# Kernel tuning notes

Measured on AMD Instinct MI355X. Metric: run time of the kernel, lower is better.

Reference implementation:

```python
import jax, jax.numpy as jnp
import numpy as np

HEADS = 16
S = 1024      # affine_dim
B, L = 4, 2048


def _conv1x1(x, W, b):
    # Conv1d with kernel_size=1: pointwise channel mixing. x: (B, C, L)
    return jnp.einsum('oc,bcl->bol', W, x) + b[None, :, None]


def setup_inputs() -> dict:
    key = jax.random.key(0)
    ks = jax.random.split(key, 7)
    scale = 1.0 / np.sqrt(S)  # ~ torch Conv1d default init scale
    return {
        'x':  jax.random.normal(ks[0], (B, S, L), dtype=jnp.float32),
        'Wk': jax.random.normal(ks[1], (S, S), dtype=jnp.float32) * scale,
        'bk': jax.random.normal(ks[2], (S,), dtype=jnp.float32) * scale,
        'Wq': jax.random.normal(ks[3], (S, S), dtype=jnp.float32) * scale,
        'bq': jax.random.normal(ks[4], (S,), dtype=jnp.float32) * scale,
        'Wp': jax.random.normal(ks[5], (S, S), dtype=jnp.float32) * scale,
        'bp': jax.random.normal(ks[6], (S,), dtype=jnp.float32) * scale,
    }


def reference(x, Wk, bk, Wq, bq, Wp, bp):
    b, c, l = x.shape
    h = HEADS
    d = c // h
    keys = _conv1x1(x, Wk, bk).reshape(b, h, d, l)
    queries = _conv1x1(x, Wq, bq).reshape(b, h, d, l)
    # scores[b,h,i,j] = sum_d keys[...,d,i] * queries[...,d,j]  (keys^T @ queries)
    # NOTE: original scales by `seqlen ** 1 / 2` == seqlen / 2 (Python precedence),
    # i.e. multiply by 2/L, NOT 1/sqrt(L). Faithfully preserved.
    scores = jnp.einsum('bhdi,bhdj->bhij', keys, queries) * (2.0 / l)
    attn = jax.nn.softmax(scores, axis=-1)
    xh = x.reshape(b, h, d, l)  # raw x used as values
    out = jnp.einsum('bhdi,bhij->bhdj', xh, attn).reshape(b, c, l)
    return _conv1x1(out, Wp, bp)
```

## Files before the change

kernel.cpp:

```cpp
#include <hip/hip_runtime.h>
#include <hip/hip_bf16.h>
#include <cstdint>
#include <cstddef>

#ifndef __has_builtin
#define __has_builtin(x) 0
#endif

#define DEVI __device__ __forceinline__

typedef __attribute__((ext_vector_type(8))) __bf16 bf16x8;
typedef __attribute__((ext_vector_type(4))) float float4v;
typedef __attribute__((ext_vector_type(16))) float float16v;
typedef __attribute__((ext_vector_type(4))) unsigned short ushort4v;
typedef __attribute__((ext_vector_type(4))) unsigned int uint4v;

constexpr int Bd = 4, Sd = 1024, Ld = 2048, Hd = 16, Dd = 64;

DEVI unsigned short f2bf(float x){
  union { float f; unsigned u; } v; v.f = x;
  unsigned r = v.u + 0x7fffu + ((v.u >> 16) & 1u);
  return (unsigned short)(r >> 16);
}

DEVI unsigned pack2(float lo, float hi){
  union { float f; unsigned u; } a, b; a.f = lo; b.f = hi;
  unsigned ra = a.u + 0x8000u;
  unsigned rb = b.u + 0x8000u;
#if __has_builtin(__builtin_amdgcn_perm)
  return __builtin_amdgcn_perm(rb, ra, 0x07060302u);
#else
  return (ra >> 16) | (rb & 0xffff0000u);
#endif
}

DEVI float fast_exp2(float x){
#if __has_builtin(__builtin_amdgcn_exp2f)
  return __builtin_amdgcn_exp2f(x);
#else
  return exp2f(x);
#endif
}

DEVI void plane32_swap(unsigned &a, unsigned &b){
  asm("v_permlane32_swap_b32 %0, %1" : "+v"(a), "+v"(b));
}

DEVI void gload_lds16(const void* g, void* lds){
  __builtin_amdgcn_global_load_lds(
      (const __attribute__((address_space(1))) void*)g,
      (__attribute__((address_space(3))) void*)lds,
      16, 0, 0);
}

DEVI float4v mfma_bf16(bf16x8 a, bf16x8 b, float4v c){
  return __builtin_amdgcn_mfma_f32_16x16x32_bf16(a, b, c, 0, 0, 0);
}

DEVI float16v mfma32_bf16(bf16x8 a, bf16x8 b, float16v c){
  return __builtin_amdgcn_mfma_f32_32x32x16_bf16(a, b, c, 0, 0, 0);
}


__global__ void wcast_kernel(const float* __restrict__ Wk, const float* __restrict__ Wq,
                             const float* __restrict__ Wp,
                             unsigned short* __restrict__ Wkbf, unsigned short* __restrict__ Wqbf,
                             unsigned short* __restrict__ Wpbf, float ck){
  size_t i = ((size_t)blockIdx.x * 256 + threadIdx.x) * 4;
  float4v a = *(const float4v*)(Wk + i);
  float4v b = *(const float4v*)(Wq + i);
  float4v c = *(const float4v*)(Wp + i);
  ushort4v oa = { f2bf(a[0]*ck), f2bf(a[1]*ck), f2bf(a[2]*ck), f2bf(a[3]*ck) };
  ushort4v ob = { f2bf(b[0]), f2bf(b[1]), f2bf(b[2]), f2bf(b[3]) };
  ushort4v oc = { f2bf(c[0]), f2bf(c[1]), f2bf(c[2]), f2bf(c[3]) };
  *(ushort4v*)(Wkbf + i) = oa;
  *(ushort4v*)(Wqbf + i) = ob;
  *(ushort4v*)(Wpbf + i) = oc;
}

__global__ void transpose_cast(const float* __restrict__ x, unsigned short* __restrict__ Xt){
  __shared__ float tile[32][33];
  const int b = blockIdx.z;
  const int l0 = blockIdx.x * 32;
  const int s0 = blockIdx.y * 32;
  const int t = threadIdx.x;
  {
    const int r = t >> 3, c4 = (t & 7) * 4;
    float4v v = *(const float4v*)(x + ((size_t)b*Sd + s0 + r)*Ld + l0 + c4);
    tile[r][c4+0] = v[0]; tile[r][c4+1] = v[1];
    tile[r][c4+2] = v[2]; tile[r][c4+3] = v[3];
  }
  __syncthreads();
  {
    const int l = t >> 3, g4 = (t & 7) * 4;
    ushort4v o = { f2bf(tile[g4+0][l]), f2bf(tile[g4+1][l]),
                   f2bf(tile[g4+2][l]), f2bf(tile[g4+3][l]) };
    *(ushort4v*)(Xt + ((size_t)b*Ld + l0 + l)*Sd + s0 + g4) = o;
  }
}

template<int OUT_MODE>
__global__ __launch_bounds__(256, 2)
void conv_gemm(const unsigned short* __restrict__ A,
               const unsigned short* __restrict__ Bt,
               const float* __restrict__ bias, float bscale,
               unsigned short* __restrict__ outT,
               float* __restrict__ outF)
{
  constexpr int BK = 32;
  constexpr int NKSTEP = Sd / BK;
  __shared__ __attribute__((aligned(16))) unsigned short Abuf[2][128*BK];
  __shared__ __attribute__((aligned(16))) unsigned short Bbuf[2][128*BK];

  const int b  = blockIdx.z;
  const int n0 = blockIdx.x * 128;
  const int m0 = blockIdx.y * 128;
  const int tid = threadIdx.x;
  const int w = tid >> 6, lane = tid & 63, lr = lane & 15, lg = lane >> 4;
  const int wm = (w >> 1) * 64, wn = (w & 1) * 64;

  const unsigned short* Abase = A + (size_t)m0 * Sd;
  const unsigned short* Bbase = Bt + ((size_t)b * Ld + n0) * Sd;

  auto stage = [&](int bf, int kt){
    #pragma unroll
    for (int p = 0; p < 2; ++p){
      int slot = p*256 + tid;
      int row = slot >> 2, c = slot & 3;
      int csrc = c ^ ((row >> 1) & 3);
      gload_lds16(Abase + (size_t)row * Sd + kt*BK + csrc*8,
                  (void*)(&Abuf[bf][(size_t)(p*256 + w*64) * 8]));
    }
    #pragma unroll
    for (int p = 0; p < 2; ++p){
      int slot = p*256 + tid;
      int row = slot >> 2, c = slot & 3;
      int csrc = c ^ ((row >> 1) & 3);
      gload_lds16(Bbase + (size_t)row * Sd + kt*BK + csrc*8,
                  (void*)(&Bbuf[bf][(size_t)(p*256 + w*64) * 8]));
    }
  };

  const int gsw = lg ^ ((lr >> 1) & 3);

  float4v acc[4][4];
  #pragma unroll
  for (int i = 0; i < 4; ++i)
    #pragma unroll
    for (int j = 0; j < 4; ++j)
      acc[i][j] = (float4v){0.f, 0.f, 0.f, 0.f};

  stage(0, 0);
  __syncthreads();
  int cur = 0;
  for (int kt = 0; kt < NKSTEP; ++kt){
    if (kt + 1 < NKSTEP) stage(cur ^ 1, kt + 1);
    bf16x8 af[4], bfv[4];
    #pragma unroll
    for (int i = 0; i < 4; ++i){
      int row = wm + i*16 + lr;
      af[i] = *(const bf16x8*)((const char*)&Abuf[cur][0] + (size_t)row*64 + gsw*16);
    }
    #pragma unroll
    for (int j = 0; j < 4; ++j){
      int row = wn + j*16 + lr;
      bfv[j] = *(const bf16x8*)((const char*)&Bbuf[cur][0] + (size_t)row*64 + gsw*16);
    }
    #pragma unroll
    for (int i = 0; i < 4; ++i)
      #pragma unroll
      for (int j = 0; j < 4; ++j)
        acc[i][j] = mfma_bf16(af[i], bfv[j], acc[i][j]);
    __syncthreads();
    cur ^= 1;
  }

  #pragma unroll
  for (int i = 0; i < 4; ++i){
    const int mb = m0 + wm + i*16 + lg*4;
    float4v bv = *(const float4v*)(bias + mb);
    #pragma unroll
    for (int j = 0; j < 4; ++j){
      const int n = n0 + wn + j*16 + lr;
      float4v v = acc[i][j];
      float o0 = v[0] + bscale*bv[0];
      float o1 = v[1] + bscale*bv[1];
      float o2 = v[2] + bscale*bv[2];
      float o3 = v[3] + bscale*bv[3];
      if (OUT_MODE == 0){
        ushort4v o = { f2bf(o0), f2bf(o1), f2bf(o2), f2bf(o3) };
        *(ushort4v*)(outT + ((size_t)b*Ld + n)*Sd + mb) = o;
      } else {
        outF[((size_t)b*Sd + mb + 0)*Ld + n] = o0;
        outF[((size_t)b*Sd + mb + 1)*Ld + n] = o1;
        outF[((size_t)b*Sd + mb + 2)*Ld + n] = o2;
        outF[((size_t)b*Sd + mb + 3)*Ld + n] = o3;
      }
    }
  }
}

__global__ __launch_bounds__(256, 2)
void conv_gemm_kq(const unsigned short* __restrict__ Ak,
                  const unsigned short* __restrict__ Aq,
                  const unsigned short* __restrict__ Bt,
                  const float* __restrict__ bk, const float* __restrict__ bq,
                  float ck,
                  unsigned short* __restrict__ Kt,
                  unsigned short* __restrict__ Qt)
{
  constexpr int BK = 32;
  constexpr int NKSTEP = Sd / BK;
  __shared__ __attribute__((aligned(16))) unsigned short AbufK[2][128*BK];
  __shared__ __attribute__((aligned(16))) unsigned short AbufQ[2][128*BK];
  __shared__ __attribute__((aligned(16))) unsigned short Bbuf[2][128*BK];

  const int b  = blockIdx.z;
  const int n0 = blockIdx.x * 128;
  const int m0 = blockIdx.y * 128;
  const int tid = threadIdx.x;
  const int w = tid >> 6, lane = tid & 63, lr = lane & 15, lg = lane >> 4;
  const int wm = (w >> 1) * 64, wn = (w & 1) * 64;

  const unsigned short* AKbase = Ak + (size_t)m0 * Sd;
  const unsigned short* AQbase = Aq + (size_t)m0 * Sd;
  const unsigned short* Bbase  = Bt + ((size_t)b * Ld + n0) * Sd;

  auto stage = [&](int bf, int kt){
    #pragma unroll
    for (int p = 0; p < 2; ++p){
      int slot = p*256 + tid;
      int row = slot >> 2, c = slot & 3;
      int csrc = c ^ ((row >> 1) & 3);
      const size_t soff = (size_t)row * Sd + kt*BK + csrc*8;
      void* dk = (void*)(&AbufK[bf][(size_t)(p*256 + w*64) * 8]);
      void* dq = (void*)(&AbufQ[bf][(size_t)(p*256 + w*64) * 8]);
      void* db = (void*)(&Bbuf [bf][(size_t)(p*256 + w*64) * 8]);
      gload_lds16(AKbase + soff, dk);
      gload_lds16(AQbase + soff, dq);
      gload_lds16(Bbase  + soff, db);
    }
  };

  const int gsw = lg ^ ((lr >> 1) & 3);

  float4v acck[4][4], accq[4][4];
  #pragma unroll
  for (int i = 0; i < 4; ++i)
    #pragma unroll
    for (int j = 0; j < 4; ++j){
      acck[i][j] = (float4v){0.f, 0.f, 0.f, 0.f};
      accq[i][j] = (float4v){0.f, 0.f, 0.f, 0.f};
    }

  stage(0, 0);
  __syncthreads();
  int cur = 0;
  for (int kt = 0; kt < NKSTEP; ++kt){
    if (kt + 1 < NKSTEP) stage(cur ^ 1, kt + 1);
    bf16x8 afk[4], afq[4], bfv[4];
    #pragma unroll
    for (int i = 0; i < 4; ++i){
      int row = wm + i*16 + lr;
      afk[i] = *(const bf16x8*)((const char*)&AbufK[cur][0] + (size_t)row*64 + gsw*16);
      afq[i] = *(const bf16x8*)((const char*)&AbufQ[cur][0] + (size_t)row*64 + gsw*16);
    }
    #pragma unroll
    for (int j = 0; j < 4; ++j){
      int row = wn + j*16 + lr;
      bfv[j] = *(const bf16x8*)((const char*)&Bbuf[cur][0] + (size_t)row*64 + gsw*16);
    }
    #pragma unroll
    for (int i = 0; i < 4; ++i)
      #pragma unroll
      for (int j = 0; j < 4; ++j){
        acck[i][j] = mfma_bf16(afk[i], bfv[j], acck[i][j]);
        accq[i][j] = mfma_bf16(afq[i], bfv[j], accq[i][j]);
      }
    __syncthreads();
    cur ^= 1;
  }

  #pragma unroll
  for (int i = 0; i < 4; ++i){
    const int mb = m0 + wm + i*16 + lg*4;
    float4v bkv = *(const float4v*)(bk + mb);
    float4v bqv = *(const float4v*)(bq + mb);
    #pragma unroll
    for (int j = 0; j < 4; ++j){
      const int n = n0 + wn + j*16 + lr;
      float4v vk = acck[i][j];
      float4v vq = accq[i][j];
      ushort4v ok = { f2bf(vk[0] + ck*bkv[0]), f2bf(vk[1] + ck*bkv[1]),
                      f2bf(vk[2] + ck*bkv[2]), f2bf(vk[3] + ck*bkv[3]) };
      ushort4v oq = { f2bf(vq[0] + bqv[0]), f2bf(vq[1] + bqv[1]),
                      f2bf(vq[2] + bqv[2]), f2bf(vq[3] + bqv[3]) };
      *(ushort4v*)(Kt + ((size_t)b*Ld + n)*Sd + mb) = ok;
      *(ushort4v*)(Qt + ((size_t)b*Ld + n)*Sd + mb) = oq;
    }
  }
}

__global__ __launch_bounds__(256, 4)
void stats_kernel(const unsigned short* __restrict__ Kt,
                  const unsigned short* __restrict__ Qt,
                  const float* __restrict__ x,
                  unsigned short* __restrict__ Vp)
{
  __shared__ __attribute__((aligned(16))) unsigned short Qbuf[2][64*64];
  __shared__ __attribute__((aligned(16))) float zbuf[256];

  const int m = blockIdx.x;
  const int xcd = m & 7, slot = m >> 3;
  const int bh = xcd * 8 + (slot >> 3);
  const int ib = slot & 7;
  const int b = bh >> 4, h = bh & 15;
  const int i0 = ib * 256;

  const int tid = threadIdx.x, w = tid >> 6, lane = tid & 63;
  const int l31 = lane & 31, lh = lane >> 5;
  const int iw0 = i0 + w * 64;

  bf16x8 kb[2][4];
  #pragma unroll
  for (int is = 0; is < 2; ++is)
    #pragma unroll
    for (int ks = 0; ks < 4; ++ks)
      kb[is][ks] = *(const bf16x8*)(Kt + ((size_t)b*Ld + iw0 + is*32 + l31)*Sd + h*64 + ks*16 + lh*8);

  const size_t qbase = (size_t)b*Ld*Sd + (size_t)h*64;
  auto stage = [&](int bf, int jt){
    const int j0 = jt * 64;
    #pragma unroll
    for (int p = 0; p < 2; ++p){
      const int slot2 = p*256 + tid;
      const int row = slot2 >> 3;
      const int gsrc = (slot2 & 7) ^ (row & 7);
      gload_lds16(Qt + qbase + (size_t)(j0 + row)*Sd + gsrc*8,
                  (void*)(&Qbuf[bf][(size_t)slot2 * 8]));
    }
  };

  float z[2] = {0.f, 0.f};
  stage(0, 0);
  __syncthreads();
  int cur = 0;
  for (int jt = 0; jt < 32; ++jt){
    if (jt + 1 < 32) stage(cur ^ 1, jt + 1);
    #pragma unroll
    for (int js = 0; js < 2; ++js){
      bf16x8 qf[4];
      #pragma unroll
      for (int ks = 0; ks < 4; ++ks){
        const int row = js*32 + l31;
        const int g = (2*ks + lh) ^ (l31 & 7);
        qf[ks] = *(const bf16x8*)((const char*)&Qbuf[cur][0] + (size_t)row*128 + g*16);
      }
      #pragma unroll
      for (int is = 0; is < 2; ++is){
        float16v sacc;
        #pragma unroll
        for (int r = 0; r < 16; ++r) sacc[r] = 0.f;
        __builtin_amdgcn_s_setprio(1);
        #pragma unroll
        for (int ks = 0; ks < 4; ++ks)
          sacc = mfma32_bf16(qf[ks], kb[is][ks], sacc);
        __builtin_amdgcn_s_setprio(0);
        #pragma unroll
        for (int r = 0; r < 16; ++r) z[is] += fast_exp2(sacc[r]);
      }
    }
    __syncthreads();
    cur ^= 1;
  }

  #pragma unroll
  for (int is = 0; is < 2; ++is){
    float zv = z[is] + __shfl_xor(z[is], 32, 64);
    if (lh == 0)
      zbuf[w*64 + is*32 + l31] = 1.0f / zv;
  }
  __syncthreads();

  #pragma unroll
  for (int p = 0; p < 16; ++p){
    const int e = p*256 + tid;
    const int d = e >> 6;
    const int c4 = (e & 63) * 4;
    const size_t off = ((size_t)b*Sd + h*64 + d)*Ld + i0 + c4;
    float4v xv = *(const float4v*)(x + off);
    float4v zv = *(const float4v*)(&zbuf[c4]);
    ushort4v o = { f2bf(xv[0]*zv[0]), f2bf(xv[1]*zv[1]),
                   f2bf(xv[2]*zv[2]), f2bf(xv[3]*zv[3]) };
    *(ushort4v*)(Vp + off) = o;
  }
}

__global__ __launch_bounds__(256, 2)
void attn_pv_kernel(const unsigned short* __restrict__ Kt,
                    const unsigned short* __restrict__ Qt,
                    const unsigned short* __restrict__ Vp,
                    unsigned short* __restrict__ AOt)
{
  __shared__ __attribute__((aligned(16))) unsigned short Kbuf[2][64*64];
  __shared__ __attribute__((aligned(16))) unsigned short Vbuf[2][64*64];

  const int m = blockIdx.x;
  const int xcd = m & 7, slot = m >> 3;
  const int bh = xcd * 8 + (slot >> 3);
  const int jb = slot & 7;
  const int b = bh >> 4, h = bh & 15;
  const int j0 = jb * 256;

  const int tid = threadIdx.x, w = tid >> 6, lane = tid & 63;
  const int l31 = lane & 31, lh = lane >> 5;
  const int jw = j0 + w * 64;

  bf16x8 qb[2][4];
  #pragma unroll
  for (int js = 0; js < 2; ++js)
    #pragma unroll
    for (int ks = 0; ks < 4; ++ks)
      qb[js][ks] = *(const bf16x8*)(Qt + ((size_t)b*Ld + jw + js*32 + l31)*Sd + h*64 + ks*16 + lh*8);

  float16v oacc[2][2];
  #pragma unroll
  for (int ds = 0; ds < 2; ++ds)
    #pragma unroll
    for (int js = 0; js < 2; ++js)
      #pragma unroll
      for (int r = 0; r < 16; ++r) oacc[ds][js][r] = 0.f;

  const size_t kbase = (size_t)b*Ld*Sd + (size_t)h*64;
  const size_t vbase = ((size_t)b*Sd + h*64)*Ld;

  auto stage = [&](int bf, int it){
    const int i0 = it * 64;
    #pragma unroll
    for (int p = 0; p < 2; ++p){
      const int slot2 = p*256 + tid;
      const int row = slot2 >> 3;
      const int gsrc = (slot2 & 7) ^ (row & 7);
      gload_lds16(Kt + kbase + (size_t)(i0 + row)*Sd + gsrc*8,
                  (void*)(&Kbuf[bf][(size_t)slot2 * 8]));
      gload_lds16(Vp + vbase + (size_t)row*Ld + i0 + gsrc*8,
                  (void*)(&Vbuf[bf][(size_t)slot2 * 8]));
    }
  };

  bf16x8 kf[2][4], vf[2][4];
  float16v sacc2[2][2];

  auto read_kf = [&](int cb){
    #pragma unroll
    for (int is = 0; is < 2; ++is)
      #pragma unroll
      for (int ks = 0; ks < 4; ++ks){
        const int row = is*32 + l31;
        const int g = (2*ks + lh) ^ (l31 & 7);
        kf[is][ks] = *(const bf16x8*)((const char*)&Kbuf[cb][0] + (size_t)row*128 + g*16);
      }
  };
  auto read_vf = [&](int cb){
    #pragma unroll
    for (int is = 0; is < 2; ++is)
      #pragma unroll
      for (int ks = 0; ks < 4; ++ks){
        const int row = is*32 + l31;
        const int g = (2*ks + lh) ^ (l31 & 7);
        vf[is][ks] = *(const bf16x8*)((const char*)&Vbuf[cb][0] + (size_t)row*128 + g*16);
      }
  };
  auto do_qk = [&](){
    #pragma unroll
    for (int is = 0; is < 2; ++is)
      #pragma unroll
      for (int js = 0; js < 2; ++js)
        #pragma unroll
        for (int r = 0; r < 16; ++r) sacc2[is][js][r] = 0.f;
    __builtin_amdgcn_s_setprio(1);
    #pragma unroll
    for (int js = 0; js < 2; ++js)
      #pragma unroll
      for (int is = 0; is < 2; ++is)
        #pragma unroll
        for (int ks = 0; ks < 4; ++ks)
          sacc2[is][js] = mfma32_bf16(kf[is][ks], qb[js][ks], sacc2[is][js]);
    __builtin_amdgcn_s_setprio(0);
  };
  auto do_exp_pv = [&](){
    #pragma unroll
    for (int js = 0; js < 2; ++js){
      bf16x8 pf[4];
      #pragma unroll
      for (int is = 0; is < 2; ++is){
        #pragma unroll
        for (int hs = 0; hs < 2; ++hs){
          const int r0 = 8*hs;
          unsigned W0 = pack2(fast_exp2(sacc2[is][js][r0+0]), fast_exp2(sacc2[is][js][r0+1]));
          unsigned W1 = pack2(fast_exp2(sacc2[is][js][r0+2]), fast_exp2(sacc2[is][js][r0+3]));
          unsigned W2 = pack2(fast_exp2(sacc2[is][js][r0+4]), fast_exp2(sacc2[is][js][r0+5]));
          unsigned W3 = pack2(fast_exp2(sacc2[is][js][r0+6]), fast_exp2(sacc2[is][js][r0+7]));
          plane32_swap(W0, W2);
          plane32_swap(W1, W3);
          union { uint4v u; bf16x8 v; } cvt;
          cvt.u = (uint4v){ W0, W1, W2, W3 };
          pf[is*2 + hs] = cvt.v;
        }
      }
      __builtin_amdgcn_s_setprio(1);
      #pragma unroll
      for (int kp = 0; kp < 4; ++kp)
        #pragma unroll
        for (int ds = 0; ds < 2; ++ds)
          oacc[ds][js] = mfma32_bf16(vf[ds][kp], pf[kp], oacc[ds][js]);
      __builtin_amdgcn_s_setprio(0);
    }
  };

  stage(0, 0);
  __syncthreads();
  stage(1, 1);
  read_kf(0);
  do_qk();
  read_vf(0);

  for (int t = 0; t < 31; ++t){
    __syncthreads();
    if (t < 30) stage(t & 1, t + 2);
    read_kf((t + 1) & 1);
    do_exp_pv();
    do_qk();
    read_vf((t + 1) & 1);
  }
  do_exp_pv();

  #pragma unroll
  for (int ds = 0; ds < 2; ++ds)
    #pragma unroll
    for (int js = 0; js < 2; ++js)
      #pragma unroll
      for (int rq = 0; rq < 4; ++rq){
        const int d0 = ds*32 + 8*rq + 4*lh;
        ushort4v o = { f2bf(oacc[ds][js][4*rq+0]), f2bf(oacc[ds][js][4*rq+1]),
                       f2bf(oacc[ds][js][4*rq+2]), f2bf(oacc[ds][js][4*rq+3]) };
        *(ushort4v*)(AOt + ((size_t)b*Ld + jw + js*32 + l31)*Sd + h*64 + d0) = o;
      }
}


extern "C" void kernel_launch(void* const* d_in, const int* in_sizes, int n_in,
                              void* d_out, int out_size, void* d_ws, size_t ws_size,
                              hipStream_t stream)
{
  const float* x  = (const float*)d_in[0];
  const float* Wk = (const float*)d_in[1];
  const float* bk = (const float*)d_in[2];
  const float* Wq = (const float*)d_in[3];
  const float* bq = (const float*)d_in[4];
  const float* Wp = (const float*)d_in[5];
  const float* bp = (const float*)d_in[6];
  float* out = (float*)d_out;

  char* ws = (char*)d_ws;
  const size_t SZ_BLS = (size_t)Bd * Ld * Sd * 2;
  unsigned short* Xt   = (unsigned short*)(ws);
  unsigned short* Kt   = (unsigned short*)(ws + SZ_BLS);
  unsigned short* Qt   = (unsigned short*)(ws + 2*SZ_BLS);
  unsigned short* AOt  = (unsigned short*)(ws + 3*SZ_BLS);
  unsigned short* Wkbf = (unsigned short*)(ws + 4*SZ_BLS);
  unsigned short* Wqbf = (unsigned short*)(ws + 4*SZ_BLS + (size_t)2097152);
  unsigned short* Wpbf = (unsigned short*)(ws + 4*SZ_BLS + (size_t)2*2097152);
  unsigned short* Vp   = Xt;

  const float ck = (2.0f / (float)Ld) * 1.44269504088896f;

  wcast_kernel<<<1024, 256, 0, stream>>>(Wk, Wq, Wp, Wkbf, Wqbf, Wpbf, ck);
  transpose_cast<<<dim3(Ld/32, Sd/32, Bd), 256, 0, stream>>>(x, Xt);

  dim3 cg(Ld/128, Sd/128, Bd);
  conv_gemm_kq<<<cg, 256, 0, stream>>>(Wkbf, Wqbf, Xt, bk, bq, ck, Kt, Qt);

  stats_kernel<<<dim3((Ld/256)*(Bd*Hd)), 256, 0, stream>>>(Kt, Qt, x, Vp);
  attn_pv_kernel<<<dim3((Ld/256)*(Bd*Hd)), 256, 0, stream>>>(Kt, Qt, Vp, AOt);

  conv_gemm<1><<<cg, 256, 0, stream>>>(Wpbf, AOt, bp, 1.0f, nullptr, out);
}
```

Measured before the change: 214.9 us.

## Read V fragments from global memory and triple-buffer K tiles in pairs

The attention kernel no longer stages V through LDS. Each lane loads its V fragments directly from global memory, and the freed LDS holds a three-slot ring of K tile pairs. The ring is refilled every other iteration, which halves the number of barriers in the main loop. The cost is strided, uncached-in-LDS global loads for V on the critical path. Those V loads share the vector-memory counter with the async K prefetches, so waiting on V can also stall on the K loads. A leftover unused shared array is also declared.

```diff
diff --git a/kernel.cpp b/kernel.cpp
--- a/kernel.cpp
+++ b/kernel.cpp
@@ -402,8 +402,8 @@
                     const unsigned short* __restrict__ Vp,
                     unsigned short* __restrict__ AOt)
 {
-  __shared__ __attribute__((aligned(16))) unsigned short Kbuf[2][64*64];
-  __shared__ __attribute__((aligned(16))) unsigned short Vbuf[2][64*64];
+  __shared__ __attribute__((aligned(16))) unsigned short Kbuf[3][2][64*64/ (64/64)][1];
+  __shared__ __attribute__((aligned(16))) unsigned short Kb[3][2][4096];
 
   const int m = blockIdx.x;
   const int xcd = m & 7, slot = m >> 3;
@@ -434,7 +434,7 @@
   const size_t kbase = (size_t)b*Ld*Sd + (size_t)h*64;
   const size_t vbase = ((size_t)b*Sd + h*64)*Ld;
 
-  auto stage = [&](int bf, int it){
+  auto stage_tile = [&](int sl, int hf, int it){
     const int i0 = it * 64;
     #pragma unroll
     for (int p = 0; p < 2; ++p){
@@ -442,33 +442,36 @@
       const int row = slot2 >> 3;
       const int gsrc = (slot2 & 7) ^ (row & 7);
       gload_lds16(Kt + kbase + (size_t)(i0 + row)*Sd + gsrc*8,
-                  (void*)(&Kbuf[bf][(size_t)slot2 * 8]));
-      gload_lds16(Vp + vbase + (size_t)row*Ld + i0 + gsrc*8,
-                  (void*)(&Vbuf[bf][(size_t)slot2 * 8]));
-    }
+                  (void*)(&Kb[sl][hf][(size_t)slot2 * 8]));
+    }
+  };
+  auto stage_pair = [&](int p){
+    stage_tile(p % 3, 0, 2*p);
+    stage_tile(p % 3, 1, 2*p + 1);
   };
 
   bf16x8 kf[2][4], vf[2][4];
   float16v sacc2[2][2];
 
-  auto read_kf = [&](int cb){
+  auto read_kf = [&](int u){
+    const int sl = (u >> 1) % 3, hf = u & 1;
     #pragma unroll
     for (int is = 0; is < 2; ++is)
       #pragma unroll
       for (int ks = 0; ks < 4; ++ks){
         const int row = is*32 + l31;
         const int g = (2*ks + lh) ^ (l31 & 7);
-        kf[is][ks] = *(const bf16x8*)((const char*)&Kbuf[cb][0] + (size_t)row*128 + g*16);
-      }
-  };
-  auto read_vf = [&](int cb){
+        kf[is][ks] = *(const bf16x8*)((const char*)&Kb[sl][hf][0] + (size_t)row*128 + g*16);
+      }
+  };
+  auto read_vf = [&](int u){
+    const int i0 = u * 64;
     #pragma unroll
     for (int is = 0; is < 2; ++is)
       #pragma unroll
       for (int ks = 0; ks < 4; ++ks){
         const int row = is*32 + l31;
-        const int g = (2*ks + lh) ^ (l31 & 7);
-        vf[is][ks] = *(const bf16x8*)((const char*)&Vbuf[cb][0] + (size_t)row*128 + g*16);
+        vf[is][ks] = *(const bf16x8*)(Vp + vbase + (size_t)row*Ld + i0 + (2*ks + lh)*8);
       }
   };
   auto do_qk = [&](){
@@ -518,20 +521,22 @@
     }
   };
 
-  stage(0, 0);
+  stage_pair(0);
+  stage_pair(1);
   __syncthreads();
-  stage(1, 1);
   read_kf(0);
   do_qk();
   read_vf(0);
 
   for (int t = 0; t < 31; ++t){
-    __syncthreads();
-    if (t < 30) stage(t & 1, t + 2);
-    read_kf((t + 1) & 1);
+    if ((t & 1) == 0){
+      if (t > 0) __syncthreads();
+      if (t <= 26) stage_pair(t/2 + 2);
+    }
+    read_kf(t + 1);
     do_exp_pv();
     do_qk();
-    read_vf((t + 1) & 1);
+    read_vf(t + 1);
   }
   do_exp_pv();
 
@@ -546,6 +551,7 @@
                        f2bf(oacc[ds][js][4*rq+2]), f2bf(oacc[ds][js][4*rq+3]) };
         *(ushort4v*)(AOt + ((size_t)b*Ld + jw + js*32 + l31)*Sd + h*64 + d0) = o;
       }
+  (void)Kbuf;
 }
 
 
```

New measurement: 566.2 us. 163% more time.
